# Kernel tuning notes

Hardware: AMD Instinct MI355X
Metric: run time of the kernel (lower is better)

## Reference

```python
import jax, jax.numpy as jnp
import numpy as np
from math import sqrt

D = 128
HEADS = 16
N = 8192


def setup_inputs() -> dict:
    key = jax.random.key(0)
    ks = jax.random.split(key, 11)
    s = 0.02
    dh = D * HEADS
    return {
        "q": jax.random.normal(ks[0], (N, D), dtype=jnp.float32),
        "k": jax.random.normal(ks[1], (N, D), dtype=jnp.float32),
        "v": jax.random.normal(ks[2], (N, D), dtype=jnp.float32),
        "Wq": jax.random.normal(ks[3], (D, dh), dtype=jnp.float32) * s,
        "bq": jax.random.normal(ks[4], (dh,), dtype=jnp.float32) * s,
        "Wk": jax.random.normal(ks[5], (D, dh), dtype=jnp.float32) * s,
        "bk": jax.random.normal(ks[6], (dh,), dtype=jnp.float32) * s,
        "Wv": jax.random.normal(ks[7], (D, dh), dtype=jnp.float32) * s,
        "bv": jax.random.normal(ks[8], (dh,), dtype=jnp.float32) * s,
        "Wo": jax.random.normal(ks[9], (dh, D), dtype=jnp.float32) * s,
        "bo": jax.random.normal(ks[10], (D,), dtype=jnp.float32) * s,
    }


def reference(q, k, v, Wq, bq, Wk, bk, Wv, bv, Wo, bo):
    # Projections to d*heads, then view as [N, d, heads]
    # (torch .view(-1, d, heads): feature index f = i*heads + h)
    q3 = (q @ Wq + bq).reshape(-1, D, HEADS)
    k3 = (k @ Wk + bk).reshape(-1, D, HEADS)
    v3 = (v @ Wv + bv).reshape(-1, D, HEADS)
    # Per-token scores over the feature dim: [N, d, d]
    scores = jnp.einsum("nih,njh->nij", q3, k3) / sqrt(D)
    # Faithful to original: softmax over dim 1 (NOT the last dim)
    attn = jax.nn.softmax(scores, axis=1)
    out3 = jnp.einsum("nij,njh->nih", attn, v3)  # [N, d, heads]
    out = out3.reshape(-1, HEADS * D)  # same row-major layout as torch reshape
    return out @ Wo + bo  # [N, d]
```

## Files before the change

### kernel.cpp

```cpp
#include <hip/hip_runtime.h>
#include <hip/hip_bf16.h>
#include <stdint.h>


#define NTOK 8192
#define DDIM 128
#define DH   2048

typedef float   f32x16 __attribute__((ext_vector_type(16)));
typedef __bf16  bf16x8 __attribute__((ext_vector_type(8)));
typedef uint32_t u32x4 __attribute__((ext_vector_type(4)));

static __device__ __forceinline__ uint32_t cvt_pk_bf16(float lo, float hi) {
  uint32_t r;
  asm("v_cvt_pk_bf16_f32 %0, %1, %2" : "=v"(r) : "v"(lo), "v"(hi));
  return r;
}
static __device__ __forceinline__ int crow4(int r, int hi) {
  return (r & 3) + 8 * (r >> 2) + 4 * hi;
}
template <int CTRL>
static __device__ __forceinline__ float dpp_add(float s) {
  int t = __builtin_amdgcn_update_dpp(0, __builtin_bit_cast(int, s), CTRL, 0xf, 0xf, true);
  return s + __builtin_bit_cast(float, t);
}

__global__ __launch_bounds__(256) void prep_weights(
    const float* __restrict__ Wq, const float* __restrict__ Wk,
    const float* __restrict__ Wv, const float* __restrict__ Wo,
    uint16_t* __restrict__ WqT, uint16_t* __restrict__ WkT,
    uint16_t* __restrict__ WvT, uint16_t* __restrict__ WoT) {
  const int t = threadIdx.x, bx = blockIdx.x, z = blockIdx.y;
  if (z < 3) {
    const float* W = (z == 0) ? Wq : (z == 1) ? Wk : Wv;
    uint16_t* WT = (z == 0) ? WqT : (z == 1) ? WkT : WvT;
    const int col = bx * 256 + t;
    const int g = col >> 5, il = col & 31;
    for (int kc = 0; kc < 16; ++kc) {
      u32x4 wv;
      #pragma unroll
      for (int p = 0; p < 4; ++p) {
        float f0 = W[(size_t)(kc * 8 + 2 * p) * DH + col];
        float f1 = W[(size_t)(kc * 8 + 2 * p + 1) * DH + col];
        wv[p] = cvt_pk_bf16(f0, f1);
      }
      *(u32x4*)(WT + (size_t)g * 4096 + (kc >> 1) * 512 + (kc & 1) * 256 + il * 8) = wv;
    }
  } else {
    const int col = t & 127, ksub = t >> 7;
    const int kbase = bx * 256 + ksub * 128;
    for (int kc = 0; kc < 16; ++kc) {
      const int k0 = kbase + kc * 8;
      u32x4 wv;
      #pragma unroll
      for (int p = 0; p < 4; ++p) {
        float f0 = Wo[(size_t)(k0 + 2 * p) * DDIM + col];
        float f1 = Wo[(size_t)(k0 + 2 * p + 1) * DDIM + col];
        wv[p] = cvt_pk_bf16(f0, f1);
      }
      *(u32x4*)(WoT + (size_t)col * DH + k0) = wv;
    }
  }
}

__global__ __launch_bounds__(256, 3) void proj_kernel(
    const float* __restrict__ q, const float* __restrict__ kin,
    const float* __restrict__ v,
    const uint16_t* __restrict__ WqT, const uint16_t* __restrict__ WkT,
    const uint16_t* __restrict__ WvT,
    const float* __restrict__ bq, const float* __restrict__ bk,
    const float* __restrict__ bv,
    uint16_t* __restrict__ q3, uint16_t* __restrict__ k3,
    uint16_t* __restrict__ v3) {
  __shared__ uint16_t astage[4096];
  __shared__ uint16_t tile[32 * 512];
  const int z = blockIdx.z;
  const float* A = (z == 0) ? q : (z == 1) ? kin : v;
  const uint16_t* WTf = (z == 0) ? WqT : (z == 1) ? WkT : WvT;
  const float* bias = (z == 0) ? bq : (z == 1) ? bk : bv;
  uint16_t* dst = (z == 0) ? q3 : (z == 1) ? k3 : v3;
  const bool vlayout = (z == 2);
  const float CEXP = 1.4426950408889634f * 0.08838834764831845f;
  const float cs = (z == 0) ? CEXP : 1.0f;

  const int t = threadIdx.x;
  const int w = t >> 6, l = t & 63;
  const int il = l & 31, hi = l >> 5;
  const int T = blockIdx.x, by = blockIdx.y;
  const int rowbase = T * 32;

  {
    const int rp = t >> 3, kc = t & 7;
    const float* ap = A + ((size_t)rowbase + rp) * DDIM + kc * 16;
    float4 f0 = *(const float4*)(ap + 0);
    float4 f1 = *(const float4*)(ap + 4);
    float4 f2 = *(const float4*)(ap + 8);
    float4 f3 = *(const float4*)(ap + 12);
    u32x4 u0 = { cvt_pk_bf16(f0.x, f0.y), cvt_pk_bf16(f0.z, f0.w),
                 cvt_pk_bf16(f1.x, f1.y), cvt_pk_bf16(f1.z, f1.w) };
    u32x4 u1 = { cvt_pk_bf16(f2.x, f2.y), cvt_pk_bf16(f2.z, f2.w),
                 cvt_pk_bf16(f3.x, f3.y), cvt_pk_bf16(f3.z, f3.w) };
    *(u32x4*)(astage + kc * 512 + rp * 8) = u0;
    *(u32x4*)(astage + kc * 512 + 256 + rp * 8) = u1;
  }
  __syncthreads();

  const int lo = hi * 256 + il * 8;
  bf16x8 af[8];
  #pragma unroll
  for (int ks = 0; ks < 8; ++ks)
    af[ks] = *(const bf16x8*)(astage + ks * 512 + lo);

  const uint16_t* WB = WTf + (size_t)(by * 16 + w * 4) * 4096;
  f32x16 acc0 = {}, acc1 = {}, acc2 = {}, acc3 = {};
  #pragma unroll
  for (int ks = 0; ks < 8; ++ks) {
    bf16x8 b0 = *(const bf16x8*)(WB + 0 * 4096 + ks * 512 + lo);
    bf16x8 b1 = *(const bf16x8*)(WB + 1 * 4096 + ks * 512 + lo);
    bf16x8 b2 = *(const bf16x8*)(WB + 2 * 4096 + ks * 512 + lo);
    bf16x8 b3 = *(const bf16x8*)(WB + 3 * 4096 + ks * 512 + lo);
    acc0 = __builtin_amdgcn_mfma_f32_32x32x16_bf16(af[ks], b0, acc0, 0, 0, 0);
    acc1 = __builtin_amdgcn_mfma_f32_32x32x16_bf16(af[ks], b1, acc1, 0, 0, 0);
    acc2 = __builtin_amdgcn_mfma_f32_32x32x16_bf16(af[ks], b2, acc2, 0, 0, 0);
    acc3 = __builtin_amdgcn_mfma_f32_32x32x16_bf16(af[ks], b3, acc3, 0, 0, 0);
  }

  #pragma unroll
  for (int nt = 0; nt < 4; ++nt) {
    const f32x16 acc = (nt == 0) ? acc0 : (nt == 1) ? acc1 : (nt == 2) ? acc2 : acc3;
    const int lc = w * 128 + nt * 32 + il;
    const float bval = bias[by * 512 + lc];
    int cm;
    if (!vlayout) {
      const int c = (lc >> 3) & 1;
      cm = (c * 256 + (lc >> 4) * 8 + (lc & 7)) ^ (c << 4);
    } else {
      cm = ((lc >> 7) & 3) * 128 + (lc & 15) * 8 + ((lc >> 4) & 7);
    }
    #pragma unroll
    for (int r = 0; r < 16; r += 2) {
      const int rr0 = crow4(r, hi);
      const uint32_t pk = cvt_pk_bf16((acc[r] + bval) * cs, (acc[r + 1] + bval) * cs);
      tile[rr0 * 512 + cm] = (uint16_t)pk;
      tile[(rr0 + 1) * 512 + cm] = (uint16_t)(pk >> 16);
    }
  }
  __syncthreads();

  #pragma unroll
  for (int kk2 = 0; kk2 < 8; ++kk2) {
    const int u = t + kk2 * 256;
    const int rr = u >> 6, qq = u & 63;
    int toff;
    size_t gaddr;
    const size_t n = rowbase + rr;
    if (!vlayout) {
      toff = (qq * 8) ^ ((qq >> 5) << 4);
      gaddr = n * 2048 + (size_t)(qq >> 5) * 1024 + (size_t)by * 256 + (qq & 31) * 8;
    } else {
      toff = qq * 8;
      gaddr = n * 2048 + (size_t)by * 512 + (size_t)(qq >> 4) * 128 + (qq & 15) * 8;
    }
    u32x4 val = *(const u32x4*)(tile + rr * 512 + toff);
    *(u32x4*)(dst + gaddr) = val;
  }
}

__global__ __launch_bounds__(256) void attn_kernel(
    const uint16_t* q3, const uint16_t* __restrict__ k3,
    const uint16_t* __restrict__ v3, uint16_t* out3) {
  __shared__ float part[4 * 2048];
  const int n = blockIdx.x;
  const int w = threadIdx.x >> 6;
  const int l = threadIdx.x & 63;
  const int il = l & 31, hi = l >> 5;
  const uint16_t* qb = q3 + (size_t)n * 2048;
  const uint16_t* kb = k3 + (size_t)n * 2048;
  const uint16_t* vb = v3 + (size_t)n * 2048;

  bf16x8 af = *(const bf16x8*)(kb + hi * 1024 + (size_t)(w * 32 + il) * 8);
  bf16x8 vf0 = *(const bf16x8*)(vb + (size_t)(w * 4 + hi) * 128 + (il & 15) * 8);
  bf16x8 vf1 = *(const bf16x8*)(vb + (size_t)(w * 4 + hi + 2) * 128 + (il & 15) * 8);
  f32x16 d0 = {}, d1 = {}, d2 = {}, d3 = {};
  {
    bf16x8 bq0 = *(const bf16x8*)(qb + hi * 1024 + (size_t)(0 * 32 + il) * 8);
    bf16x8 bq1 = *(const bf16x8*)(qb + hi * 1024 + (size_t)(1 * 32 + il) * 8);
    bf16x8 bq2 = *(const bf16x8*)(qb + hi * 1024 + (size_t)(2 * 32 + il) * 8);
    bf16x8 bq3 = *(const bf16x8*)(qb + hi * 1024 + (size_t)(3 * 32 + il) * 8);
    d0 = __builtin_amdgcn_mfma_f32_32x32x16_bf16(af, bq0, d0, 0, 0, 0);
    d1 = __builtin_amdgcn_mfma_f32_32x32x16_bf16(af, bq1, d1, 0, 0, 0);
    d2 = __builtin_amdgcn_mfma_f32_32x32x16_bf16(af, bq2, d2, 0, 0, 0);
    d3 = __builtin_amdgcn_mfma_f32_32x32x16_bf16(af, bq3, d3, 0, 0, 0);
  }
  #pragma unroll
  for (int r = 0; r < 16; ++r) {
    float e0 = exp2f(d0[r]), e1 = exp2f(d1[r]);
    float e2 = exp2f(d2[r]), e3 = exp2f(d3[r]);
    float s = (e0 + e1) + (e2 + e3);
    s = dpp_add<0xB1>(s);
    s = dpp_add<0x4E>(s);
    s = dpp_add<0x124>(s);
    s = dpp_add<0x128>(s);
    s += __shfl_xor(s, 16);
    const float rs = __builtin_amdgcn_rcpf(s);
    d0[r] = e0 * rs; d1[r] = e1 * rs; d2[r] = e2 * rs; d3[r] = e3 * rs;
  }
  #pragma unroll
  for (int mi = 0; mi < 4; ++mi) {
    const f32x16 p = (mi == 0) ? d0 : (mi == 1) ? d1 : (mi == 2) ? d2 : d3;
    uint32_t pk0 = cvt_pk_bf16(p[0],  p[1]),  pk1 = cvt_pk_bf16(p[2],  p[3]);
    uint32_t pk2 = cvt_pk_bf16(p[4],  p[5]),  pk3 = cvt_pk_bf16(p[6],  p[7]);
    uint32_t pk4 = cvt_pk_bf16(p[8],  p[9]),  pk5 = cvt_pk_bf16(p[10], p[11]);
    uint32_t pk6 = cvt_pk_bf16(p[12], p[13]), pk7 = cvt_pk_bf16(p[14], p[15]);
    auto sA = __builtin_amdgcn_permlane32_swap(pk0, pk2, false, false);
    auto sB = __builtin_amdgcn_permlane32_swap(pk1, pk3, false, false);
    auto sC = __builtin_amdgcn_permlane32_swap(pk4, pk6, false, false);
    auto sD = __builtin_amdgcn_permlane32_swap(pk5, pk7, false, false);
    u32x4 fw0 = { sA[0], sB[0], sA[1], sB[1] };
    u32x4 fw1 = { sC[0], sD[0], sC[1], sD[1] };
    f32x16 oz = {};
    oz = __builtin_amdgcn_mfma_f32_32x32x16_bf16(__builtin_bit_cast(bf16x8, fw0), vf0, oz, 0, 0, 0);
    oz = __builtin_amdgcn_mfma_f32_32x32x16_bf16(__builtin_bit_cast(bf16x8, fw1), vf1, oz, 0, 0, 0);
    if (il < 16) {
      #pragma unroll
      for (int r = 0; r < 16; r += 2) {
        const int i = mi * 32 + crow4(r, hi);
        float2 val = { oz[r], oz[r + 1] };
        *(float2*)&part[w * 2048 + il * 128 + (i ^ ((il & 7) << 2))] = val;
      }
    }
  }
  __syncthreads();
  const int t = threadIdx.x;
  const int i0 = t >> 1, h0 = (t & 1) * 8;
  float sv[8];
  #pragma unroll
  for (int e = 0; e < 8; ++e) {
    const int idx = (h0 + e) * 128 + (i0 ^ (((h0 + e) & 7) << 2));
    sv[e] = (part[idx] + part[2048 + idx]) + (part[4096 + idx] + part[6144 + idx]);
  }
  u32x4 ov = { cvt_pk_bf16(sv[0], sv[1]), cvt_pk_bf16(sv[2], sv[3]),
               cvt_pk_bf16(sv[4], sv[5]), cvt_pk_bf16(sv[6], sv[7]) };
  *(u32x4*)(out3 + (size_t)n * 2048 + t * 8) = ov;
}

__global__ __launch_bounds__(512) void outproj_kernel(
    const uint16_t* __restrict__ out3, const uint16_t* __restrict__ WoT,
    const float* __restrict__ bo, float* __restrict__ out) {
  __shared__ float part[4][32][32];
  const int w = threadIdx.x >> 6;
  const int l = threadIdx.x & 63;
  const int il = l & 31, hi = l >> 5;
  const int nt = w >> 1, ksv = w & 1;
  const int rowbase = blockIdx.x * 32;
  f32x16 acc = {};
  #pragma unroll 4
  for (int kb = 0; kb < 64; ++kb) {
    const int kk = ksv * 1024 + kb * 16 + hi * 8;
    bf16x8 afr = *(const bf16x8*)(out3 + (size_t)(rowbase + il) * DH + kk);
    bf16x8 bfr = *(const bf16x8*)(WoT + (size_t)(nt * 32 + il) * DH + kk);
    acc = __builtin_amdgcn_mfma_f32_32x32x16_bf16(afr, bfr, acc, 0, 0, 0);
  }
  if (ksv == 1) {
    #pragma unroll
    for (int r = 0; r < 16; ++r) part[nt][crow4(r, hi)][il] = acc[r];
  }
  __syncthreads();
  if (ksv == 0) {
    const int col = nt * 32 + il;
    const float bval = bo[col];
    #pragma unroll
    for (int r = 0; r < 16; ++r) {
      const int rr = crow4(r, hi);
      out[(size_t)(rowbase + rr) * DDIM + col] = acc[r] + part[nt][rr][il] + bval;
    }
  }
}

extern "C" void kernel_launch(void* const* d_in, const int* in_sizes, int n_in,
                              void* d_out, int out_size, void* d_ws, size_t ws_size,
                              hipStream_t stream) {
  (void)in_sizes; (void)n_in; (void)out_size; (void)ws_size;
  const float* q  = (const float*)d_in[0];
  const float* k  = (const float*)d_in[1];
  const float* v  = (const float*)d_in[2];
  const float* Wq = (const float*)d_in[3];
  const float* bq = (const float*)d_in[4];
  const float* Wk = (const float*)d_in[5];
  const float* bk = (const float*)d_in[6];
  const float* Wv = (const float*)d_in[7];
  const float* bv = (const float*)d_in[8];
  const float* Wo = (const float*)d_in[9];
  const float* bo = (const float*)d_in[10];
  float* out = (float*)d_out;

  char* ws = (char*)d_ws;
  const size_t MB = 1024ull * 1024ull;
  uint16_t* q3  = (uint16_t*)(ws);
  uint16_t* k3  = (uint16_t*)(ws + 32 * MB);
  uint16_t* v3  = (uint16_t*)(ws + 64 * MB);
  uint16_t* WqT = (uint16_t*)(ws + 96 * MB);
  uint16_t* WkT = WqT + (size_t)DH * 128;
  uint16_t* WvT = WkT + (size_t)DH * 128;
  uint16_t* WoT = WvT + (size_t)DH * 128;

  prep_weights<<<dim3(8, 4), 256, 0, stream>>>(Wq, Wk, Wv, Wo, WqT, WkT, WvT, WoT);
  proj_kernel<<<dim3(256, 4, 3), 256, 0, stream>>>(q, k, v, WqT, WkT, WvT,
                                                   bq, bk, bv, q3, k3, v3);
  attn_kernel<<<dim3(NTOK), 256, 0, stream>>>(q3, k3, v3, q3);
  outproj_kernel<<<dim3(256), 512, 0, stream>>>(q3, WoT, bo, out);
}
```

Baseline: 136.3 us.

## Process four tokens per attention block with prefetch and LDS-staged P·V

The attention kernel now handles four tokens per block in a loop, prefetching the next token's K/Q fragments while the current softmax runs. The P·V product is restructured so probabilities are packed to bf16 in shared memory and each wave computes its own output slice with eight MFMAs. This removes the fp32 cross-wave partial-sum reduction. It also swaps the shuffle for ds_swizzle and exp2f for raw v_exp. The cost is two barriers per token and a serial loop, which reduces the block count and the parallelism available to hide latency.

```diff
diff --git a/kernel.cpp b/kernel.cpp
--- a/kernel.cpp
+++ b/kernel.cpp
@@ -7,13 +7,20 @@
 #define DDIM 128
 #define DH   2048
 
-typedef float   f32x16 __attribute__((ext_vector_type(16)));
-typedef __bf16  bf16x8 __attribute__((ext_vector_type(8)));
-typedef uint32_t u32x4 __attribute__((ext_vector_type(4)));
+typedef float    f32x16 __attribute__((ext_vector_type(16)));
+typedef float    f32x4  __attribute__((ext_vector_type(4)));
+typedef __bf16   bf16x8 __attribute__((ext_vector_type(8)));
+typedef uint32_t u32x4  __attribute__((ext_vector_type(4)));
+typedef uint32_t u32x2  __attribute__((ext_vector_type(2)));
 
 static __device__ __forceinline__ uint32_t cvt_pk_bf16(float lo, float hi) {
   uint32_t r;
   asm("v_cvt_pk_bf16_f32 %0, %1, %2" : "=v"(r) : "v"(lo), "v"(hi));
+  return r;
+}
+static __device__ __forceinline__ float v_exp(float x) {
+  float r;
+  asm("v_exp_f32 %0, %1" : "=v"(r) : "v"(x));
   return r;
 }
 static __device__ __forceinline__ int crow4(int r, int hi) {
@@ -169,79 +176,103 @@
 __global__ __launch_bounds__(256) void attn_kernel(
     const uint16_t* q3, const uint16_t* __restrict__ k3,
     const uint16_t* __restrict__ v3, uint16_t* out3) {
-  __shared__ float part[4 * 2048];
-  const int n = blockIdx.x;
+  __shared__ uint32_t xch[8192];
   const int w = threadIdx.x >> 6;
   const int l = threadIdx.x & 63;
   const int il = l & 31, hi = l >> 5;
-  const uint16_t* qb = q3 + (size_t)n * 2048;
-  const uint16_t* kb = k3 + (size_t)n * 2048;
-  const uint16_t* vb = v3 + (size_t)n * 2048;
-
-  bf16x8 af = *(const bf16x8*)(kb + hi * 1024 + (size_t)(w * 32 + il) * 8);
-  bf16x8 vf0 = *(const bf16x8*)(vb + (size_t)(w * 4 + hi) * 128 + (il & 15) * 8);
-  bf16x8 vf1 = *(const bf16x8*)(vb + (size_t)(w * 4 + hi + 2) * 128 + (il & 15) * 8);
-  f32x16 d0 = {}, d1 = {}, d2 = {}, d3 = {};
-  {
-    bf16x8 bq0 = *(const bf16x8*)(qb + hi * 1024 + (size_t)(0 * 32 + il) * 8);
-    bf16x8 bq1 = *(const bf16x8*)(qb + hi * 1024 + (size_t)(1 * 32 + il) * 8);
-    bf16x8 bq2 = *(const bf16x8*)(qb + hi * 1024 + (size_t)(2 * 32 + il) * 8);
-    bf16x8 bq3 = *(const bf16x8*)(qb + hi * 1024 + (size_t)(3 * 32 + il) * 8);
+  const size_t n0 = (size_t)blockIdx.x * 4;
+  const uint16_t* qb = q3 + n0 * 2048;
+  const uint16_t* kb = k3 + n0 * 2048;
+  const uint16_t* vb = v3 + n0 * 2048;
+  uint16_t* ob = out3 + n0 * 2048;
+
+  const int aoff = hi * 1024 + (w * 32 + il) * 8;
+  const int boff = hi * 1024 + il * 8;
+  uint32_t* xw = xch + (w * 2048 + il * 4 + hi * 2);
+  const uint32_t* xr = xch + (w * 512 + hi * 128 + il * 4);
+
+  bf16x8 af  = *(const bf16x8*)(kb + aoff);
+  bf16x8 bq0 = *(const bf16x8*)(qb + boff + 0);
+  bf16x8 bq1 = *(const bf16x8*)(qb + boff + 256);
+  bf16x8 bq2 = *(const bf16x8*)(qb + boff + 512);
+  bf16x8 bq3 = *(const bf16x8*)(qb + boff + 768);
+
+  #pragma unroll 1
+  for (int tt = 0; tt < 4; ++tt) {
+    f32x16 d0 = {}, d1 = {}, d2 = {}, d3 = {};
     d0 = __builtin_amdgcn_mfma_f32_32x32x16_bf16(af, bq0, d0, 0, 0, 0);
     d1 = __builtin_amdgcn_mfma_f32_32x32x16_bf16(af, bq1, d1, 0, 0, 0);
     d2 = __builtin_amdgcn_mfma_f32_32x32x16_bf16(af, bq2, d2, 0, 0, 0);
     d3 = __builtin_amdgcn_mfma_f32_32x32x16_bf16(af, bq3, d3, 0, 0, 0);
-  }
-  #pragma unroll
-  for (int r = 0; r < 16; ++r) {
-    float e0 = exp2f(d0[r]), e1 = exp2f(d1[r]);
-    float e2 = exp2f(d2[r]), e3 = exp2f(d3[r]);
-    float s = (e0 + e1) + (e2 + e3);
-    s = dpp_add<0xB1>(s);
-    s = dpp_add<0x4E>(s);
-    s = dpp_add<0x124>(s);
-    s = dpp_add<0x128>(s);
-    s += __shfl_xor(s, 16);
-    const float rs = __builtin_amdgcn_rcpf(s);
-    d0[r] = e0 * rs; d1[r] = e1 * rs; d2[r] = e2 * rs; d3[r] = e3 * rs;
-  }
-  #pragma unroll
-  for (int mi = 0; mi < 4; ++mi) {
-    const f32x16 p = (mi == 0) ? d0 : (mi == 1) ? d1 : (mi == 2) ? d2 : d3;
-    uint32_t pk0 = cvt_pk_bf16(p[0],  p[1]),  pk1 = cvt_pk_bf16(p[2],  p[3]);
-    uint32_t pk2 = cvt_pk_bf16(p[4],  p[5]),  pk3 = cvt_pk_bf16(p[6],  p[7]);
-    uint32_t pk4 = cvt_pk_bf16(p[8],  p[9]),  pk5 = cvt_pk_bf16(p[10], p[11]);
-    uint32_t pk6 = cvt_pk_bf16(p[12], p[13]), pk7 = cvt_pk_bf16(p[14], p[15]);
-    auto sA = __builtin_amdgcn_permlane32_swap(pk0, pk2, false, false);
-    auto sB = __builtin_amdgcn_permlane32_swap(pk1, pk3, false, false);
-    auto sC = __builtin_amdgcn_permlane32_swap(pk4, pk6, false, false);
-    auto sD = __builtin_amdgcn_permlane32_swap(pk5, pk7, false, false);
-    u32x4 fw0 = { sA[0], sB[0], sA[1], sB[1] };
-    u32x4 fw1 = { sC[0], sD[0], sC[1], sD[1] };
-    f32x16 oz = {};
-    oz = __builtin_amdgcn_mfma_f32_32x32x16_bf16(__builtin_bit_cast(bf16x8, fw0), vf0, oz, 0, 0, 0);
-    oz = __builtin_amdgcn_mfma_f32_32x32x16_bf16(__builtin_bit_cast(bf16x8, fw1), vf1, oz, 0, 0, 0);
-    if (il < 16) {
-      #pragma unroll
-      for (int r = 0; r < 16; r += 2) {
-        const int i = mi * 32 + crow4(r, hi);
-        float2 val = { oz[r], oz[r + 1] };
-        *(float2*)&part[w * 2048 + il * 128 + (i ^ ((il & 7) << 2))] = val;
-      }
-    }
-  }
-  __syncthreads();
-  const int t = threadIdx.x;
-  const int i0 = t >> 1, h0 = (t & 1) * 8;
-  float sv[8];
-  #pragma unroll
-  for (int e = 0; e < 8; ++e) {
-    const int idx = (h0 + e) * 128 + (i0 ^ (((h0 + e) & 7) << 2));
-    sv[e] = (part[idx] + part[2048 + idx]) + (part[4096 + idx] + part[6144 + idx]);
-  }
-  u32x4 ov = { cvt_pk_bf16(sv[0], sv[1]), cvt_pk_bf16(sv[2], sv[3]),
-               cvt_pk_bf16(sv[4], sv[5]), cvt_pk_bf16(sv[6], sv[7]) };
-  *(u32x4*)(out3 + (size_t)n * 2048 + t * 8) = ov;
+    const int tn = (tt < 3) ? tt + 1 : 3;
+    bf16x8 afn = *(const bf16x8*)(kb + tn * 2048 + aoff);
+    bf16x8 bn0 = *(const bf16x8*)(qb + tn * 2048 + boff + 0);
+    bf16x8 bn1 = *(const bf16x8*)(qb + tn * 2048 + boff + 256);
+    bf16x8 bn2 = *(const bf16x8*)(qb + tn * 2048 + boff + 512);
+    bf16x8 bn3 = *(const bf16x8*)(qb + tn * 2048 + boff + 768);
+    #pragma unroll
+    for (int r = 0; r < 16; ++r) {
+      float e0 = v_exp(d0[r]), e1 = v_exp(d1[r]);
+      float e2 = v_exp(d2[r]), e3 = v_exp(d3[r]);
+      float s = (e0 + e1) + (e2 + e3);
+      s = dpp_add<0xB1>(s);
+      s = dpp_add<0x4E>(s);
+      s = dpp_add<0x124>(s);
+      s = dpp_add<0x128>(s);
+      s += __builtin_bit_cast(float,
+             __builtin_amdgcn_ds_swizzle(__builtin_bit_cast(int, s), 0x401F));
+      const float rs = __builtin_amdgcn_rcpf(s);
+      d0[r] = e0 * rs; d1[r] = e1 * rs; d2[r] = e2 * rs; d3[r] = e3 * rs;
+    }
+    #define PACK_WRITE(dm, mi_) do {                                           \
+      u32x2 q01 = { cvt_pk_bf16(dm[0],  dm[1]),  cvt_pk_bf16(dm[2],  dm[3])  };\
+      u32x2 q23 = { cvt_pk_bf16(dm[4],  dm[5]),  cvt_pk_bf16(dm[6],  dm[7])  };\
+      u32x2 q45 = { cvt_pk_bf16(dm[8],  dm[9]),  cvt_pk_bf16(dm[10], dm[11]) };\
+      u32x2 q67 = { cvt_pk_bf16(dm[12], dm[13]), cvt_pk_bf16(dm[14], dm[15]) };\
+      uint32_t* wp_ = xw + (mi_) * 512;                                        \
+      *(u32x2*)(wp_ + 0)   = q01;                                              \
+      *(u32x2*)(wp_ + 128) = q23;                                              \
+      *(u32x2*)(wp_ + 256) = q45;                                              \
+      *(u32x2*)(wp_ + 384) = q67;                                              \
+    } while (0)
+    PACK_WRITE(d0, 0); PACK_WRITE(d1, 1); PACK_WRITE(d2, 2); PACK_WRITE(d3, 3);
+    #undef PACK_WRITE
+    const uint16_t* vt = vb + tt * 2048 + (il & 15) * 8;
+    bf16x8 vf0 = *(const bf16x8*)(vt + (0 + hi) * 128);
+    bf16x8 vf1 = *(const bf16x8*)(vt + (2 + hi) * 128);
+    bf16x8 vf2 = *(const bf16x8*)(vt + (4 + hi) * 128);
+    bf16x8 vf3 = *(const bf16x8*)(vt + (6 + hi) * 128);
+    bf16x8 vf4 = *(const bf16x8*)(vt + (8 + hi) * 128);
+    bf16x8 vf5 = *(const bf16x8*)(vt + (10 + hi) * 128);
+    bf16x8 vf6 = *(const bf16x8*)(vt + (12 + hi) * 128);
+    bf16x8 vf7 = *(const bf16x8*)(vt + (14 + hi) * 128);
+    __syncthreads();
+    f32x16 ot = {};
+    u32x4 pf;
+    pf = *(const u32x4*)(xr + 0 * 2048 + 0 * 256);
+    ot = __builtin_amdgcn_mfma_f32_32x32x16_bf16(vf0, __builtin_bit_cast(bf16x8, pf), ot, 0, 0, 0);
+    pf = *(const u32x4*)(xr + 0 * 2048 + 1 * 256);
+    ot = __builtin_amdgcn_mfma_f32_32x32x16_bf16(vf1, __builtin_bit_cast(bf16x8, pf), ot, 0, 0, 0);
+    pf = *(const u32x4*)(xr + 1 * 2048 + 0 * 256);
+    ot = __builtin_amdgcn_mfma_f32_32x32x16_bf16(vf2, __builtin_bit_cast(bf16x8, pf), ot, 0, 0, 0);
+    pf = *(const u32x4*)(xr + 1 * 2048 + 1 * 256);
+    ot = __builtin_amdgcn_mfma_f32_32x32x16_bf16(vf3, __builtin_bit_cast(bf16x8, pf), ot, 0, 0, 0);
+    pf = *(const u32x4*)(xr + 2 * 2048 + 0 * 256);
+    ot = __builtin_amdgcn_mfma_f32_32x32x16_bf16(vf4, __builtin_bit_cast(bf16x8, pf), ot, 0, 0, 0);
+    pf = *(const u32x4*)(xr + 2 * 2048 + 1 * 256);
+    ot = __builtin_amdgcn_mfma_f32_32x32x16_bf16(vf5, __builtin_bit_cast(bf16x8, pf), ot, 0, 0, 0);
+    pf = *(const u32x4*)(xr + 3 * 2048 + 0 * 256);
+    ot = __builtin_amdgcn_mfma_f32_32x32x16_bf16(vf6, __builtin_bit_cast(bf16x8, pf), ot, 0, 0, 0);
+    pf = *(const u32x4*)(xr + 3 * 2048 + 1 * 256);
+    ot = __builtin_amdgcn_mfma_f32_32x32x16_bf16(vf7, __builtin_bit_cast(bf16x8, pf), ot, 0, 0, 0);
+    uint16_t* op = ob + tt * 2048 + (size_t)(w * 32 + il) * 16;
+    *(uint32_t*)(op + 4 * hi + 0)  = cvt_pk_bf16(ot[0], ot[1]);
+    *(uint32_t*)(op + 4 * hi + 2)  = cvt_pk_bf16(ot[2], ot[3]);
+    *(uint32_t*)(op + 4 * hi + 8)  = cvt_pk_bf16(ot[4], ot[5]);
+    *(uint32_t*)(op + 4 * hi + 10) = cvt_pk_bf16(ot[6], ot[7]);
+    __syncthreads();
+    af = afn; bq0 = bn0; bq1 = bn1; bq2 = bn2; bq3 = bn3;
+  }
 }
 
 __global__ __launch_bounds__(512) void outproj_kernel(
@@ -307,6 +338,6 @@
   prep_weights<<<dim3(8, 4), 256, 0, stream>>>(Wq, Wk, Wv, Wo, WqT, WkT, WvT, WoT);
   proj_kernel<<<dim3(256, 4, 3), 256, 0, stream>>>(q, k, v, WqT, WkT, WvT,
                                                    bq, bk, bv, q3, k3, v3);
-  attn_kernel<<<dim3(NTOK), 256, 0, stream>>>(q3, k3, v3, q3);
+  attn_kernel<<<dim3(2048), 256, 0, stream>>>(q3, k3, v3, q3);
   outproj_kernel<<<dim3(256), 512, 0, stream>>>(q3, WoT, bo, out);
 }
```

New measurement: 121.2 us. -11.1%, faster.
